# Optimization experiments

Measured on AMD Instinct MI355X. Metric: run time of the kernel, lower is better.

Reference implementation:

```python
import jax, jax.numpy as jnp
import numpy as np

B, N, C = 8, 1025, 1024
H = 8
D = C // H  # 128
LORA = 16
TOK = 1024

def setup_inputs() -> dict:
    key = jax.random.key(0)
    ks = jax.random.split(key, 16)
    s = 0.02
    return {
        "x": jax.random.normal(ks[0], (B, N, C), jnp.float32),
        "style_k": jax.random.normal(ks[1], (B, N, C), jnp.float32),
        "style_v": jax.random.normal(ks[2], (B, N, C), jnp.float32),
        "W_qkv": jax.random.normal(ks[3], (C, 3 * C), jnp.float32) * s,
        "W_proj": jax.random.normal(ks[4], (C, C), jnp.float32) * s,
        "b_proj": jnp.zeros((C,), jnp.float32),
        "ak": jax.random.normal(ks[5], (TOK, LORA), jnp.float32) * s,
        "bk": jax.random.normal(ks[6], (LORA, C), jnp.float32) * s,
        "av": jax.random.normal(ks[7], (TOK, LORA), jnp.float32) * s,
        "bv": jax.random.normal(ks[8], (LORA, C), jnp.float32) * s,
        "W1": jax.random.normal(ks[9], (C, C // 4), jnp.float32) * s,
        "b1": jnp.zeros((C // 4,), jnp.float32),
        "W2": jax.random.normal(ks[10], (C // 4, 1), jnp.float32) * s,
        "b2": jnp.zeros((1,), jnp.float32),
    }

def reference(x, style_k, style_v, W_qkv, W_proj, b_proj, ak, bk, av, bv, W1, b1, W2, b2):
    Bx, Nx, Cx = x.shape
    # cls-token gating MLP over transposed patch tokens: cp has shape [B, C, N-1], N-1 == C
    cls_token = x[:, :1, :]                         # [B,1,C]
    cp = jnp.transpose(x[:, 1:, :], (0, 2, 1))      # [B,C,N-1]
    h = jax.nn.relu(cp @ W1 + b1)                   # [B,C,C//4]
    attn_w = jax.nn.sigmoid(h @ W2 + b2)            # [B,C,1]
    attn_w = attn_w[..., 0][:, None, :]             # [B,1,C]
    weighted_cls = cls_token * attn_w               # [B,1,C]

    qkv = (x @ W_qkv).reshape(Bx, Nx, 3, H, D)
    q, k, v = qkv[:, :, 0], qkv[:, :, 1], qkv[:, :, 2]  # each [B,N,H,D]

    tokens_k = ak @ bk                              # [TOK, C] (TOK == C)
    tokens_v = av @ bv
    lora_k = (style_k @ tokens_k.T).reshape(Bx, Nx, H, D)
    lora_v = (style_v @ tokens_v.T).reshape(Bx, Nx, H, D)

    kk = k + lora_k
    vv = v + lora_v
    scale = D ** -0.5  # xformers default softmax scale
    scores = jnp.einsum('bqhd,bkhd->bhqk', q, kk) * scale
    attn = jax.nn.softmax(scores, axis=-1)
    out = jnp.einsum('bhqk,bkhd->bqhd', attn, vv).reshape(Bx, Nx, Cx)
    out = out @ W_proj + b_proj

    x_return = jnp.concatenate([out[:, :1, :] + weighted_cls, out[:, 1:, :]], axis=1)
    return (x_return, vv)
```

## Files before the change

### kernel.cpp

```cpp
#include <hip/hip_runtime.h>
#include <hip/hip_bf16.h>
#include <stdint.h>

#define B_ 8
#define N_ 1025
#define C_ 1024
#define H_ 8
#define D_ 128
#define TOK_ 1024
#define LORA_ 16
#define M_ 8200
#define NPAD_ 1032

using bf16x8 = __attribute__((ext_vector_type(8))) short;
using f32x4  = __attribute__((ext_vector_type(4))) float;
using f32x16 = __attribute__((ext_vector_type(16))) float;
using u32x4  = __attribute__((ext_vector_type(4))) unsigned;
typedef unsigned short u16;

__device__ __forceinline__ u16 f2bf(float f) {
    union { float f; unsigned u; } v; v.f = f;
    unsigned r = v.u + 0x7fffu + ((v.u >> 16) & 1u);
    return (u16)(r >> 16);
}

__device__ __forceinline__ unsigned cvt_pk_bf16(float lo, float hi) {
    unsigned r;
    asm("v_cvt_pk_bf16_f32 %0, %1, %2" : "=v"(r) : "v"(lo), "v"(hi));
    return r;
}

__device__ __forceinline__ void gload16(const u16* g, u16* l) {
    __builtin_amdgcn_global_load_lds(
        (const __attribute__((address_space(1))) void*)g,
        (__attribute__((address_space(3))) void*)l, 16, 0, 0);
}

__device__ __forceinline__ int xcd_swz(int bid, int nwg) {
    int cpx = nwg >> 3;
    return (bid & 7) * cpx + (bid >> 3);
}
__device__ __forceinline__ int xcd_swz_g(int bid, int nwg) {
    int q = nwg >> 3, r = nwg & 7;
    int xcd = bid & 7, i = bid >> 3;
    return (xcd < r ? xcd * (q + 1) : r * (q + 1) + (xcd - r) * q) + i;
}

__global__ __launch_bounds__(256) void cast3_kernel(
    const float* __restrict__ x, const float* __restrict__ sk, const float* __restrict__ sv,
    u16* __restrict__ xb, u16* __restrict__ skb, u16* __restrict__ svb)
{
    const float* in = blockIdx.y == 0 ? x : (blockIdx.y == 1 ? sk : sv);
    u16* out = blockIdx.y == 0 ? xb : (blockIdx.y == 1 ? skb : svb);
    size_t i = (size_t)blockIdx.x * 256 + threadIdx.x;
    float4 a = *((const float4*)in + i * 2);
    float4 b = *((const float4*)in + i * 2 + 1);
    bf16x8 v;
    v[0] = (short)f2bf(a.x); v[1] = (short)f2bf(a.y);
    v[2] = (short)f2bf(a.z); v[3] = (short)f2bf(a.w);
    v[4] = (short)f2bf(b.x); v[5] = (short)f2bf(b.y);
    v[6] = (short)f2bf(b.z); v[7] = (short)f2bf(b.w);
    *(bf16x8*)(out + i * 8) = v;
}

__global__ __launch_bounds__(256) void padcast16_kernel(
    const float* __restrict__ ak, const float* __restrict__ av,
    u16* __restrict__ akp, u16* __restrict__ avp)
{
    const float* in = blockIdx.y ? av : ak;
    u16* out = blockIdx.y ? avp : akp;
    int i = blockIdx.x * 256 + threadIdx.x;
    int t = i >> 4, l = i & 15;
    out[(size_t)t * 32 + l] = f2bf(in[i]);
    out[(size_t)t * 32 + 16 + l] = 0;
}

__global__ __launch_bounds__(256) void castb_kernel(
    const float* __restrict__ bk, const float* __restrict__ bv,
    u16* __restrict__ bkb, u16* __restrict__ bvb)
{
    const float* in = blockIdx.y ? bv : bk;
    u16* out = blockIdx.y ? bvb : bkb;
    int i = blockIdx.x * 256 + threadIdx.x;
    out[i] = f2bf(in[i]);
}

__global__ __launch_bounds__(256) void lora16_mfma(
    const u16* __restrict__ skb, const u16* __restrict__ svb,
    const u16* __restrict__ bkb, const u16* __restrict__ bvb,
    u16* __restrict__ sk16p, u16* __restrict__ sv16p)
{
    const u16* sb = blockIdx.y ? svb : skb;
    const u16* bb = blockIdx.y ? bvb : bkb;
    u16* op = blockIdx.y ? sv16p : sk16p;
    const int lane = threadIdx.x & 63, wid = threadIdx.x >> 6;
    const int base = blockIdx.x * 64 + wid * 16;
    int ma = base + (lane & 15); if (ma > M_ - 1) ma = M_ - 1;
    const int l = lane & 15;
    const u16* arow = sb + (size_t)ma * C_ + (lane >> 4) * 8;
    const u16* brow = bb + (size_t)l * C_ + (lane >> 4) * 8;
    f32x4 acc = {0.f, 0.f, 0.f, 0.f};
#pragma unroll
    for (int k0 = 0; k0 < C_; k0 += 32) {
        bf16x8 af = *(const bf16x8*)(arow + k0);
        bf16x8 bf = *(const bf16x8*)(brow + k0);
        acc = __builtin_amdgcn_mfma_f32_16x16x32_bf16(af, bf, acc, 0, 0, 0);
    }
#pragma unroll
    for (int r = 0; r < 4; ++r) {
        int m = base + (lane >> 4) * 4 + r; if (m > M_ - 1) m = M_ - 1;
        op[(size_t)m * 32 + l] = f2bf(acc[r]);
        op[(size_t)m * 32 + 16 + l] = 0;
    }
}

__global__ __launch_bounds__(256) void wt_kernel(
    const float* __restrict__ in, u16* __restrict__ out, int K, int Nw)
{
    __shared__ float t[32][33];
    int n0 = blockIdx.x * 32, k0 = blockIdx.y * 32;
    int tx = threadIdx.x & 31, ty = threadIdx.x >> 5;
#pragma unroll
    for (int yy = 0; yy < 32; yy += 8)
        t[ty + yy][tx] = in[(size_t)(k0 + ty + yy) * Nw + n0 + tx];
    __syncthreads();
#pragma unroll
    for (int yy = 0; yy < 32; yy += 8)
        out[(size_t)(n0 + ty + yy) * K + k0 + tx] = f2bf(t[tx][ty + yy]);
}

__global__ __launch_bounds__(256) void xt_kernel(
    const float* __restrict__ x, u16* __restrict__ xT)
{
    __shared__ float tb[32][33];
    int t0 = blockIdx.x * 32, c0 = blockIdx.y * 32, b = blockIdx.z;
    int tx = threadIdx.x & 31, ty = threadIdx.x >> 5;
#pragma unroll
    for (int yy = 0; yy < 32; yy += 8)
        tb[ty + yy][tx] = x[((size_t)b * N_ + 1 + t0 + ty + yy) * C_ + c0 + tx];
    __syncthreads();
#pragma unroll
    for (int yy = 0; yy < 32; yy += 8)
        xT[((size_t)b * 1024 + c0 + ty + yy) * 1024 + t0 + tx] = f2bf(tb[tx][ty + yy]);
}

__global__ __launch_bounds__(256) void vvt_kernel(
    const float* __restrict__ vv, u16* __restrict__ vvT)
{
    __shared__ float t[32][33];
    int n0 = blockIdx.x * 32, d0 = blockIdx.y * 32, bh = blockIdx.z;
    int b = bh >> 3, h = bh & 7;
    int tx = threadIdx.x & 31, ty = threadIdx.x >> 5;
#pragma unroll
    for (int yy = 0; yy < 32; yy += 8) {
        int n = n0 + ty + yy; if (n > 1024) n = 1024;
        t[ty + yy][tx] = vv[((size_t)(b * N_) + n) * C_ + h * D_ + d0 + tx];
    }
    __syncthreads();
#pragma unroll
    for (int yy = 0; yy < 32; yy += 8) {
        int n = n0 + tx;
        if (n < NPAD_)
            vvT[((size_t)bh * D_ + d0 + ty + yy) * NPAD_ + n] = f2bf(t[tx][ty + yy]);
    }
}

__device__ __forceinline__ void stage_tile(
    const u16* __restrict__ base, int row0, int maxrow,
    u16* lds, int k0, int lane, int wid)
{
#pragma unroll
    for (int j = 0; j < 4; ++j) {
        int i = wid * 4 + j;
        int p = i * 1024 + 16 * lane;
        int row = p >> 7, cb = p & 127;
        int cbs = cb ^ ((row & 7) << 4);
        int gr = row0 + row; if (gr > maxrow) gr = maxrow;
        gload16(base + (size_t)gr * 1024 + k0 + (cbs >> 1), lds + i * 512);
    }
}

__device__ __forceinline__ void gemm_pass(
    const u16* __restrict__ A, const u16* __restrict__ Bt, int row0, int nb0,
    u16* As, u16* Bs, f32x4 acc[4][4],
    const int lane, const int wid, const int wr, const int wc)
{
    for (int k0 = 0; k0 < 1024; k0 += 64) {
        __syncthreads();
        stage_tile(A,  row0, M_ - 1,    As, k0, lane, wid);
        stage_tile(Bt, nb0,  (1 << 30), Bs, k0, lane, wid);
        __syncthreads();
#pragma unroll
        for (int ks = 0; ks < 2; ++ks) {
            bf16x8 af[4], bfr[4];
#pragma unroll
            for (int mi = 0; mi < 4; ++mi) {
                int r = wr * 64 + mi * 16 + (lane & 15);
                int byte = (r * 128 + ks * 64 + (lane >> 4) * 16) ^ ((r & 7) << 4);
                af[mi] = *(const bf16x8*)((const char*)As + byte);
            }
#pragma unroll
            for (int ni = 0; ni < 4; ++ni) {
                int r = wc * 64 + ni * 16 + (lane & 15);
                int byte = (r * 128 + ks * 64 + (lane >> 4) * 16) ^ ((r & 7) << 4);
                bfr[ni] = *(const bf16x8*)((const char*)Bs + byte);
            }
#pragma unroll
            for (int mi = 0; mi < 4; ++mi)
#pragma unroll
                for (int ni = 0; ni < 4; ++ni)
                    acc[mi][ni] = __builtin_amdgcn_mfma_f32_16x16x32_bf16(
                        af[mi], bfr[ni], acc[mi][ni], 0, 0, 0);
        }
    }
}

template<int NSEG>
__device__ __forceinline__ void stage_tile512(
    const u16* __restrict__ base, int row0, int maxrow,
    u16* lds, int k0, int lane, int wid)
{
#pragma unroll
    for (int j = 0; j < NSEG; ++j) {
        int i = wid * NSEG + j;
        int p = i * 1024 + 16 * lane;
        int row = p >> 7, cb = p & 127;
        int cbs = cb ^ ((row & 7) << 4);
        int gr = row0 + row; if (gr > maxrow) gr = maxrow;
        gload16(base + (size_t)gr * 1024 + k0 + (cbs >> 1), lds + i * 512);
    }
}

__device__ __forceinline__ void gemm_pass512(
    const u16* __restrict__ A, const u16* __restrict__ Bt, int row0, int nb0,
    u16* As, u16* Bs, f32x4 acc[4][4],
    const int lane, const int wid, const int wr, const int wc)
{
    for (int k0 = 0; k0 < 1024; k0 += 64) {
        __syncthreads();
        stage_tile512<2>(A,  row0, M_ - 1,    As, k0, lane, wid);
        stage_tile512<4>(Bt, nb0,  (1 << 30), Bs, k0, lane, wid);
        __syncthreads();
#pragma unroll
        for (int ks = 0; ks < 2; ++ks) {
            bf16x8 af[4], bfr[4];
#pragma unroll
            for (int mi = 0; mi < 4; ++mi) {
                int r = wr * 64 + mi * 16 + (lane & 15);
                int byte = (r * 128 + ks * 64 + (lane >> 4) * 16) ^ ((r & 7) << 4);
                af[mi] = *(const bf16x8*)((const char*)As + byte);
            }
#pragma unroll
            for (int ni = 0; ni < 4; ++ni) {
                int r = wc * 64 + ni * 16 + (lane & 15);
                int byte = (r * 128 + ks * 64 + (lane >> 4) * 16) ^ ((r & 7) << 4);
                bfr[ni] = *(const bf16x8*)((const char*)Bs + byte);
            }
#pragma unroll
            for (int mi = 0; mi < 4; ++mi)
#pragma unroll
                for (int ni = 0; ni < 4; ++ni)
                    acc[mi][ni] = __builtin_amdgcn_mfma_f32_16x16x32_bf16(
                        af[mi], bfr[ni], acc[mi][ni], 0, 0, 0);
        }
    }
}

__global__ __launch_bounds__(256) void se_gemm(
    const u16* __restrict__ xT, const u16* __restrict__ W1T,
    const float* __restrict__ b1, const float* __restrict__ W2,
    float* __restrict__ gred)
{
    __shared__ u16 As[8192], Bs[8192];
    __shared__ float red[128];
    const int tid = threadIdx.x, lane = tid & 63, wid = tid >> 6;
    const int wr = wid >> 1, wc = wid & 1;
    const int row0 = blockIdx.x * 128;
    const int pass = blockIdx.y;
    if (tid < 128) red[tid] = 0.f;
    const f32x4 FZ = {0.f, 0.f, 0.f, 0.f};

    f32x4 acc[4][4];
#pragma unroll
    for (int mi = 0; mi < 4; ++mi)
#pragma unroll
        for (int ni = 0; ni < 4; ++ni) acc[mi][ni] = FZ;
    gemm_pass(xT, W1T, row0, pass * 128, As, Bs, acc, lane, wid, wr, wc);
#pragma unroll
    for (int mi = 0; mi < 4; ++mi) {
#pragma unroll
        for (int r = 0; r < 4; ++r) {
            float v = 0.f;
#pragma unroll
            for (int ni = 0; ni < 4; ++ni) {
                int j = pass * 128 + wc * 64 + ni * 16 + (lane & 15);
                float h = acc[mi][ni][r] + b1[j];
                v += fmaxf(h, 0.f) * W2[j];
            }
#pragma unroll
            for (int off = 1; off < 16; off <<= 1) v += __shfl_xor(v, off);
            if ((lane & 15) == 0)
                atomicAdd(&red[wr * 64 + mi * 16 + (lane >> 4) * 4 + r], v);
        }
    }
    __syncthreads();
    if (tid < 128) atomicAdd(&gred[row0 + tid], red[tid]);
}

__global__ __launch_bounds__(256) void se_fin(
    const float* __restrict__ gred, const float* __restrict__ b2,
    const float* __restrict__ x, float* __restrict__ wcls)
{
    int row = blockIdx.x * 256 + threadIdx.x;
    int b = row >> 10, c = row & 1023;
    wcls[row] = x[(size_t)b * N_ * C_ + c] / (1.f + expf(-(gred[row] + b2[0])));
}

__global__ __launch_bounds__(512) void qkv_gemm(
    const u16* __restrict__ xb, const u16* __restrict__ WqkvT,
    const u16* __restrict__ sk16p, const u16* __restrict__ sv16p,
    const u16* __restrict__ akp, const u16* __restrict__ avp,
    u16* __restrict__ qb, u16* __restrict__ kkb, float* __restrict__ vvout)
{
    __shared__ u16 As[8192], Bs[16384];
    const int tid = threadIdx.x, lane = tid & 63, wid = tid >> 6;
    const int wr = wid >> 2, wc = wid & 3;
    const int swz = xcd_swz_g(blockIdx.x, 65 * 12);
    const int row0 = (swz / 12) * 128;
    const int ct = swz % 12, region = ct >> 2;
    const int creg = (ct & 3) * 256;
    const f32x4 FZ = {0.f, 0.f, 0.f, 0.f};
    f32x4 acc[4][4];
#pragma unroll
    for (int mi = 0; mi < 4; ++mi)
#pragma unroll
        for (int ni = 0; ni < 4; ++ni) acc[mi][ni] = FZ;

    gemm_pass512(xb, WqkvT, row0, region * 1024 + creg, As, Bs, acc, lane, wid, wr, wc);

    if (region >= 1) {
        const u16* a16 = (region == 1) ? sk16p : sv16p;
        const u16* b16 = (region == 1) ? akp : avp;
        bf16x8 af2[4], bf2v[4];
#pragma unroll
        for (int mi = 0; mi < 4; ++mi) {
            int gr = row0 + wr * 64 + mi * 16 + (lane & 15);
            if (gr > M_ - 1) gr = M_ - 1;
            af2[mi] = *(const bf16x8*)(a16 + (size_t)gr * 32 + (lane >> 4) * 8);
        }
#pragma unroll
        for (int ni = 0; ni < 4; ++ni) {
            int gc = creg + wc * 64 + ni * 16 + (lane & 15);
            bf2v[ni] = *(const bf16x8*)(b16 + (size_t)gc * 32 + (lane >> 4) * 8);
        }
#pragma unroll
        for (int mi = 0; mi < 4; ++mi)
#pragma unroll
            for (int ni = 0; ni < 4; ++ni)
                acc[mi][ni] = __builtin_amdgcn_mfma_f32_16x16x32_bf16(
                    af2[mi], bf2v[ni], acc[mi][ni], 0, 0, 0);
    }

    const float QSCALE = 0.1275006182f;
#pragma unroll
    for (int mi = 0; mi < 4; ++mi) {
#pragma unroll
        for (int r = 0; r < 4; ++r) {
            int gr = row0 + wr * 64 + mi * 16 + (lane >> 4) * 4 + r;
            if (gr >= M_) continue;
#pragma unroll
            for (int ni = 0; ni < 4; ++ni) {
                int gc = creg + wc * 64 + ni * 16 + (lane & 15);
                float v = acc[mi][ni][r];
                if (region == 0)      qb [(size_t)gr * C_ + gc] = f2bf(v * QSCALE);
                else if (region == 1) kkb[(size_t)gr * C_ + gc] = f2bf(v);
                else                  vvout[(size_t)gr * C_ + gc] = v;
            }
        }
    }
}

__global__ __launch_bounds__(512) void proj_gemm(
    const u16* __restrict__ ob, const u16* __restrict__ WprojT,
    const float* __restrict__ bias, const float* __restrict__ wcls,
    float* __restrict__ outp)
{
    __shared__ u16 As[8192], Bs[16384];
    const int tid = threadIdx.x, lane = tid & 63, wid = tid >> 6;
    const int wr = wid >> 2, wc = wid & 3;
    const int swz = xcd_swz_g(blockIdx.x, 65 * 4);
    const int row0 = (swz / 4) * 128;
    const int ct = swz % 4;
    const f32x4 FZ = {0.f, 0.f, 0.f, 0.f};
    f32x4 acc[4][4];
#pragma unroll
    for (int mi = 0; mi < 4; ++mi)
#pragma unroll
        for (int ni = 0; ni < 4; ++ni) acc[mi][ni] = FZ;

    gemm_pass512(ob, WprojT, row0, ct * 256, As, Bs, acc, lane, wid, wr, wc);

#pragma unroll
    for (int mi = 0; mi < 4; ++mi) {
#pragma unroll
        for (int r = 0; r < 4; ++r) {
            int gr = row0 + wr * 64 + mi * 16 + (lane >> 4) * 4 + r;
            if (gr >= M_) continue;
#pragma unroll
            for (int ni = 0; ni < 4; ++ni) {
                int gc = ct * 256 + wc * 64 + ni * 16 + (lane & 15);
                float v = acc[mi][ni][r] + bias[gc];
                if (gr % N_ == 0) v += wcls[(gr / N_) * C_ + gc];
                outp[(size_t)gr * C_ + gc] = v;
            }
        }
    }
}

__global__ __launch_bounds__(256) void attn_kernel(
    const u16* __restrict__ qb, const u16* __restrict__ kkb,
    const u16* __restrict__ vvT, u16* __restrict__ ob)
{
    __shared__ u16 Ks[8192];
    __shared__ u16 Vs[8192];
    const int tid = threadIdx.x, lane = tid & 63, wid = tid >> 6;
    const int swz = xcd_swz(blockIdx.x, 9 * 64);
    const int qt = swz % 9, bh = swz / 9, b = bh >> 3, h = bh & 7;
    const int n0q = qt * 128 + wid * 32;
    const int l31 = lane & 31, hi = lane >> 5;
    const float THR = 11.54f;
    const u16* kbase = kkb + (size_t)b * N_ * C_ + h * D_;
    const u16* vbase = vvT + (size_t)bh * D_ * NPAD_;

    bf16x8 qfB[8];
    {
        int qrow = n0q + l31; if (qrow > 1024) qrow = 1024;
        const u16* qp = qb + (size_t)(b * N_ + qrow) * C_ + h * D_ + hi * 8;
#pragma unroll
        for (int s = 0; s < 8; ++s) qfB[s] = *(const bf16x8*)(qp + s * 16);
    }

    const int rowK = wid * 16 + (lane >> 4);
    const int swzK = ((lane & 15) * 16) ^ ((lane >> 4) << 4);
    const u16* kp0 = kbase + (size_t)rowK * C_ + (swzK >> 1);
    const u16* kp1 = kbase + (size_t)(rowK + 4) * C_ + ((swzK ^ 64) >> 1);
    const u16* kp2 = kbase + (size_t)(rowK + 8) * C_ + ((swzK ^ 32) >> 1);
    const u16* kp3 = kbase + (size_t)(rowK + 12) * C_ + ((swzK ^ 96) >> 1);
    const int rowV = wid * 32 + (lane >> 3);
    const int swzV = ((lane & 7) * 16) ^ ((lane >> 3) << 4);
    const u16* vp0 = vbase + (size_t)rowV * NPAD_ + (swzV >> 1);
    const u16* vp1 = vbase + (size_t)(rowV + 8) * NPAD_ + ((swzV ^ 32) >> 1);

    f32x16 of[4];
#pragma unroll
    for (int i = 0; i < 16; ++i) { of[0][i] = 0.f; of[1][i] = 0.f; of[2][i] = 0.f; of[3][i] = 0.f; }
    float mrow = -3e38f, lsum = 0.f;

    u16* KsW = Ks + (size_t)wid * 4 * 512;
    u16* VsW = Vs + (size_t)wid * 4 * 512;

    for (int t = 0; t < 17; ++t) {
        __syncthreads();
        gload16(kp0, KsW);        gload16(kp1, KsW + 512);
        gload16(kp2, KsW + 1024); gload16(kp3, KsW + 1536);
        gload16(vp0, VsW);                gload16(vp1, VsW + 512);
        gload16(vp0 + 16 * NPAD_, VsW + 1024); gload16(vp1 + 16 * NPAD_, VsW + 1536);
        kp0 += 64 * C_; kp1 += 64 * C_; kp2 += 64 * C_; kp3 += 64 * C_;
        vp0 += 64; vp1 += 64;
        __syncthreads();

        f32x16 s0, s1;
#pragma unroll
        for (int i = 0; i < 16; ++i) { s0[i] = 0.f; s1[i] = 0.f; }
        const int kswz = ((l31 & 7) << 4) ^ ((l31 & 8) << 2);
        __builtin_amdgcn_s_setprio(1);
#pragma unroll
        for (int sl = 0; sl < 8; ++sl) {
            int ka = (l31 * 256 + sl * 32 + hi * 16) ^ kswz;
            bf16x8 kf0 = *(const bf16x8*)((const char*)Ks + ka);
            bf16x8 kf1 = *(const bf16x8*)((const char*)Ks + ka + 8192);
            s0 = __builtin_amdgcn_mfma_f32_32x32x16_bf16(kf0, qfB[sl], s0, 0, 0, 0);
            s1 = __builtin_amdgcn_mfma_f32_32x32x16_bf16(kf1, qfB[sl], s1, 0, 0, 0);
        }
        __builtin_amdgcn_s_setprio(0);

        if (t == 16) {
            const float NEG = -3e38f;
            s0[0] = hi ? NEG : s0[0];
#pragma unroll
            for (int r = 1; r < 16; ++r) s0[r] = NEG;
#pragma unroll
            for (int r = 0; r < 16; ++r) s1[r] = NEG;
        }

        float mt = fmaxf(s0[0], s1[0]);
#pragma unroll
        for (int r = 1; r < 16; ++r) mt = fmaxf(mt, fmaxf(s0[r], s1[r]));
        mt = fmaxf(mt, __shfl_xor(mt, 32));

        if (__any(mt > mrow + THR)) {
            float mn = fmaxf(mrow, mt);
            float al = exp2f(mrow - mn);
            mrow = mn;
            lsum *= al;
            float alr[16];
#pragma unroll
            for (int r = 0; r < 16; ++r)
                alr[r] = __shfl(al, (r & 3) + 8 * (r >> 2) + 4 * hi);
#pragma unroll
            for (int r = 0; r < 16; ++r) {
                of[0][r] *= alr[r]; of[1][r] *= alr[r];
                of[2][r] *= alr[r]; of[3][r] *= alr[r];
            }
        }
#pragma unroll
        for (int r = 0; r < 16; ++r) { s0[r] = exp2f(s0[r] - mrow); s1[r] = exp2f(s1[r] - mrow); }

        {
            float ps = 0.f;
#pragma unroll
            for (int r = 0; r < 16; ++r) ps += s0[r] + s1[r];
            ps += __shfl_xor(ps, 32);
            lsum += ps;
        }

        __builtin_amdgcn_s_setprio(1);
#pragma unroll
        for (int sub = 0; sub < 2; ++sub) {
            const f32x16& sv_ = sub ? s1 : s0;
            unsigned pk[4][2], xp[4][2];
#pragma unroll
            for (int g = 0; g < 4; ++g) {
                pk[g][0] = cvt_pk_bf16(sv_[4 * g], sv_[4 * g + 1]);
                pk[g][1] = cvt_pk_bf16(sv_[4 * g + 2], sv_[4 * g + 3]);
            }
#pragma unroll
            for (int g = 0; g < 4; ++g) {
                xp[g][0] = __shfl_xor((int)pk[g][0], 32);
                xp[g][1] = __shfl_xor((int)pk[g][1], 32);
            }
            u32x4 f0 = { hi ? xp[1][0] : pk[0][0], hi ? xp[1][1] : pk[0][1],
                         hi ? pk[1][0] : xp[0][0], hi ? pk[1][1] : xp[0][1] };
            u32x4 f1 = { hi ? xp[3][0] : pk[2][0], hi ? xp[3][1] : pk[2][1],
                         hi ? pk[3][0] : xp[2][0], hi ? pk[3][1] : xp[2][1] };
            bf16x8 pa0 = __builtin_bit_cast(bf16x8, f0);
            bf16x8 pa1 = __builtin_bit_cast(bf16x8, f1);
            const int ksl0 = sub * 2, ksl1 = sub * 2 + 1;
#pragma unroll
            for (int dsub = 0; dsub < 4; ++dsub) {
                int va0 = ((dsub * 32 + l31) * 128 + ksl0 * 32 + hi * 16) ^ kswz;
                bf16x8 vf0 = *(const bf16x8*)((const char*)Vs + va0);
                of[dsub] = __builtin_amdgcn_mfma_f32_32x32x16_bf16(pa0, vf0, of[dsub], 0, 0, 0);
            }
#pragma unroll
            for (int dsub = 0; dsub < 4; ++dsub) {
                int va1 = ((dsub * 32 + l31) * 128 + ksl1 * 32 + hi * 16) ^ kswz;
                bf16x8 vf1 = *(const bf16x8*)((const char*)Vs + va1);
                of[dsub] = __builtin_amdgcn_mfma_f32_32x32x16_bf16(pa1, vf1, of[dsub], 0, 0, 0);
            }
        }
        __builtin_amdgcn_s_setprio(0);
    }

    float invl[16];
#pragma unroll
    for (int r = 0; r < 16; ++r)
        invl[r] = 1.f / __shfl(lsum, (r & 3) + 8 * (r >> 2) + 4 * hi);
#pragma unroll
    for (int dsub = 0; dsub < 4; ++dsub)
#pragma unroll
        for (int r = 0; r < 16; ++r) {
            int n = n0q + (r & 3) + 8 * (r >> 2) + 4 * hi;
            if (n <= 1024)
                ob[(size_t)(b * N_ + n) * C_ + h * D_ + dsub * 32 + l31] =
                    f2bf(of[dsub][r] * invl[r]);
        }
}

extern "C" void kernel_launch(void* const* d_in, const int* in_sizes, int n_in,
                              void* d_out, int out_size, void* d_ws, size_t ws_size,
                              hipStream_t stream)
{
    const float* x       = (const float*)d_in[0];
    const float* style_k = (const float*)d_in[1];
    const float* style_v = (const float*)d_in[2];
    const float* W_qkv   = (const float*)d_in[3];
    const float* W_proj  = (const float*)d_in[4];
    const float* b_proj  = (const float*)d_in[5];
    const float* ak      = (const float*)d_in[6];
    const float* bk      = (const float*)d_in[7];
    const float* av      = (const float*)d_in[8];
    const float* bv      = (const float*)d_in[9];
    const float* W1      = (const float*)d_in[10];
    const float* b1      = (const float*)d_in[11];
    const float* W2      = (const float*)d_in[12];
    const float* b2      = (const float*)d_in[13];

    float* outp   = (float*)d_out;
    float* vv_out = outp + (size_t)M_ * C_;

    u16* WqkvT = (u16*)outp;
    u16* xbb   = WqkvT + (size_t)3072 * 1024;
    u16* W1T   = xbb + (size_t)M_ * C_;
    u16* akp   = W1T + (size_t)256 * 1024;
    u16* avp   = akp + 1024 * 32;
    u16* bkb   = avp + 1024 * 32;
    u16* bvb   = bkb + 16 * 1024;
    u16* sk16p = bvb + 16 * 1024;
    u16* sv16p = sk16p + (size_t)M_ * 32;

    u16* ws     = (u16*)d_ws;
    u16* qb     = ws;
    u16* kkb    = qb  + (size_t)M_ * C_;
    u16* obuf   = kkb + (size_t)M_ * C_;
    u16* vvT    = obuf + (size_t)M_ * C_;
    u16* WprojT = vvT + (size_t)B_ * H_ * D_ * NPAD_;
    float* wcls = (float*)(WprojT + (size_t)1024 * 1024);
    float* gred = wcls + 8192;
    u16* skb = obuf;
    u16* svb = vvT;
    u16* xT  = qb;

    wt_kernel<<<dim3(96, 32), 256, 0, stream>>>(W_qkv, WqkvT, 1024, 3072);
    wt_kernel<<<dim3(32, 32), 256, 0, stream>>>(W_proj, WprojT, 1024, 1024);
    wt_kernel<<<dim3(8, 32), 256, 0, stream>>>(W1, W1T, 1024, 256);
    padcast16_kernel<<<dim3(64, 2), 256, 0, stream>>>(ak, av, akp, avp);
    castb_kernel<<<dim3(64, 2), 256, 0, stream>>>(bk, bv, bkb, bvb);
    cast3_kernel<<<dim3(4100, 3), 256, 0, stream>>>(x, style_k, style_v, xbb, skb, svb);
    xt_kernel<<<dim3(32, 32, 8), 256, 0, stream>>>(x, xT);
    hipMemsetAsync(gred, 0, 8192 * sizeof(float), stream);
    se_gemm<<<dim3(64, 2), 256, 0, stream>>>(xT, W1T, b1, W2, gred);
    se_fin<<<dim3(32), 256, 0, stream>>>(gred, b2, x, wcls);
    lora16_mfma<<<dim3(129, 2), 256, 0, stream>>>(skb, svb, bkb, bvb, sk16p, sv16p);

    qkv_gemm<<<dim3(65 * 12), 512, 0, stream>>>(xbb, WqkvT, sk16p, sv16p, akp, avp,
                                                qb, kkb, vv_out);
    vvt_kernel<<<dim3(33, 4, 64), 256, 0, stream>>>(vv_out, vvT);
    attn_kernel<<<dim3(9 * 64), 256, 0, stream>>>(qb, kkb, vvT, obuf);
    proj_gemm<<<dim3(65 * 4), 512, 0, stream>>>(obuf, WprojT, b_proj, wcls, outp);
}
```

Baseline: 323.4 us.

## Double-buffer K/V tiles in attention kernel with async prefetch

Makes the K and V shared-memory tiles in the attention kernel double-buffered. The next tile's global-to-LDS loads are issued before computing on the current one, with explicit waitcnt and barriers replacing the two __syncthreads per iteration. The goal is to hide global load latency behind the MFMA work. It doubles LDS use to 64 KB per block, which may reduce occupancy, and the hand-written vmcnt counting has to match the number of loads in flight.

```diff
diff --git a/kernel.cpp b/kernel.cpp
--- a/kernel.cpp
+++ b/kernel.cpp
@@ -421,8 +421,8 @@
     const u16* __restrict__ qb, const u16* __restrict__ kkb,
     const u16* __restrict__ vvT, u16* __restrict__ ob)
 {
-    __shared__ u16 Ks[8192];
-    __shared__ u16 Vs[8192];
+    __shared__ u16 Ks[2][8192];
+    __shared__ u16 Vs[2][8192];
     const int tid = threadIdx.x, lane = tid & 63, wid = tid >> 6;
     const int swz = xcd_swz(blockIdx.x, 9 * 64);
     const int qt = swz % 9, bh = swz / 9, b = bh >> 3, h = bh & 7;
@@ -456,18 +456,40 @@
     for (int i = 0; i < 16; ++i) { of[0][i] = 0.f; of[1][i] = 0.f; of[2][i] = 0.f; of[3][i] = 0.f; }
     float mrow = -3e38f, lsum = 0.f;
 
-    u16* KsW = Ks + (size_t)wid * 4 * 512;
-    u16* VsW = Vs + (size_t)wid * 4 * 512;
+    u16* KsW0 = Ks[0] + (size_t)wid * 4 * 512;
+    u16* VsW0 = Vs[0] + (size_t)wid * 4 * 512;
+    u16* KsW1 = Ks[1] + (size_t)wid * 4 * 512;
+    u16* VsW1 = Vs[1] + (size_t)wid * 4 * 512;
+
+    gload16(kp0, KsW0);        gload16(kp1, KsW0 + 512);
+    gload16(kp2, KsW0 + 1024); gload16(kp3, KsW0 + 1536);
+    gload16(vp0, VsW0);                gload16(vp1, VsW0 + 512);
+    gload16(vp0 + 16 * NPAD_, VsW0 + 1024); gload16(vp1 + 16 * NPAD_, VsW0 + 1536);
+    kp0 += 64 * C_; kp1 += 64 * C_; kp2 += 64 * C_; kp3 += 64 * C_;
+    vp0 += 64; vp1 += 64;
 
     for (int t = 0; t < 17; ++t) {
-        __syncthreads();
-        gload16(kp0, KsW);        gload16(kp1, KsW + 512);
-        gload16(kp2, KsW + 1024); gload16(kp3, KsW + 1536);
-        gload16(vp0, VsW);                gload16(vp1, VsW + 512);
-        gload16(vp0 + 16 * NPAD_, VsW + 1024); gload16(vp1 + 16 * NPAD_, VsW + 1536);
-        kp0 += 64 * C_; kp1 += 64 * C_; kp2 += 64 * C_; kp3 += 64 * C_;
-        vp0 += 64; vp1 += 64;
-        __syncthreads();
+        const int cur = t & 1;
+        asm volatile("s_waitcnt lgkmcnt(0)" ::: "memory");
+        __builtin_amdgcn_s_barrier();
+        if (t < 16) {
+            u16* KsN = cur ? KsW0 : KsW1;
+            u16* VsN = cur ? VsW0 : VsW1;
+            gload16(kp0, KsN);        gload16(kp1, KsN + 512);
+            gload16(kp2, KsN + 1024); gload16(kp3, KsN + 1536);
+            gload16(vp0, VsN);                gload16(vp1, VsN + 512);
+            gload16(vp0 + 16 * NPAD_, VsN + 1024); gload16(vp1 + 16 * NPAD_, VsN + 1536);
+            kp0 += 64 * C_; kp1 += 64 * C_; kp2 += 64 * C_; kp3 += 64 * C_;
+            vp0 += 64; vp1 += 64;
+            asm volatile("s_waitcnt vmcnt(8)" ::: "memory");
+        } else {
+            asm volatile("s_waitcnt vmcnt(0)" ::: "memory");
+        }
+        __builtin_amdgcn_s_barrier();
+        __builtin_amdgcn_sched_barrier(0);
+
+        const u16* KsC = cur ? Ks[1] : Ks[0];
+        const u16* VsC = cur ? Vs[1] : Vs[0];
 
         f32x16 s0, s1;
 #pragma unroll
@@ -477,8 +499,8 @@
 #pragma unroll
         for (int sl = 0; sl < 8; ++sl) {
             int ka = (l31 * 256 + sl * 32 + hi * 16) ^ kswz;
-            bf16x8 kf0 = *(const bf16x8*)((const char*)Ks + ka);
-            bf16x8 kf1 = *(const bf16x8*)((const char*)Ks + ka + 8192);
+            bf16x8 kf0 = *(const bf16x8*)((const char*)KsC + ka);
+            bf16x8 kf1 = *(const bf16x8*)((const char*)KsC + ka + 8192);
             s0 = __builtin_amdgcn_mfma_f32_32x32x16_bf16(kf0, qfB[sl], s0, 0, 0, 0);
             s1 = __builtin_amdgcn_mfma_f32_32x32x16_bf16(kf1, qfB[sl], s1, 0, 0, 0);
         }
@@ -549,13 +571,13 @@
 #pragma unroll
             for (int dsub = 0; dsub < 4; ++dsub) {
                 int va0 = ((dsub * 32 + l31) * 128 + ksl0 * 32 + hi * 16) ^ kswz;
-                bf16x8 vf0 = *(const bf16x8*)((const char*)Vs + va0);
+                bf16x8 vf0 = *(const bf16x8*)((const char*)VsC + va0);
                 of[dsub] = __builtin_amdgcn_mfma_f32_32x32x16_bf16(pa0, vf0, of[dsub], 0, 0, 0);
             }
 #pragma unroll
             for (int dsub = 0; dsub < 4; ++dsub) {
                 int va1 = ((dsub * 32 + l31) * 128 + ksl1 * 32 + hi * 16) ^ kswz;
-                bf16x8 vf1 = *(const bf16x8*)((const char*)Vs + va1);
+                bf16x8 vf1 = *(const bf16x8*)((const char*)VsC + va1);
                 of[dsub] = __builtin_amdgcn_mfma_f32_32x32x16_bf16(pa1, vf1, of[dsub], 0, 0, 0);
             }
         }
```

New measurement: 331.1 us. 2.4% more time.
